# Kernel tuning notes

Measured on AMD Instinct MI355X. Metric: run time of the kernel, lower is better.

## Reference

```python
import jax, jax.numpy as jnp
import numpy as np

DIM = 2048
INNER = 8192
EPS_RMS = 1e-6
EPS_Q = 1e-5


def simple_rms_norm(x, dim):
    # x / sqrt(mean(x^2) + eps) * dim**-0.5
    rms = jnp.sqrt(jnp.mean(x * x, axis=-1, keepdims=True) + EPS_RMS)
    return x / rms * (dim ** -0.5)


def activation_quant(x):
    # per-token 8-bit quant over the last dim
    scale = 127.0 / jnp.clip(jnp.max(jnp.abs(x), axis=-1, keepdims=True), EPS_Q)
    return jnp.clip(jnp.round(x * scale), -128, 127) / scale


def weight_quant(w):
    # sign(w) * E[|w|]  (ternary since sign(0)=0)
    return jnp.sign(w) * jnp.mean(jnp.abs(w))


def bit_linear(x, w, b, dim_in):
    x_norm = simple_rms_norm(x, dim_in)
    x_q = activation_quant(x_norm)   # forward value (STE only matters for grads)
    w_q = weight_quant(w)
    return jnp.einsum('bsd,od->bso', x_q, w_q) + b


def setup_inputs() -> dict:
    key = jax.random.key(0)
    k1, k2, k3, k4, k5 = jax.random.split(key, 5)
    bound1 = 1.0 / np.sqrt(DIM)
    bound2 = 1.0 / np.sqrt(INNER)
    return {
        'x': jax.random.normal(k1, (4, 2048, DIM), dtype=jnp.float32),
        'w1': jax.random.uniform(k2, (INNER, DIM), jnp.float32, -bound1, bound1),
        'b1': jax.random.uniform(k3, (INNER,), jnp.float32, -bound1, bound1),
        'w2': jax.random.uniform(k4, (DIM, INNER), jnp.float32, -bound2, bound2),
        'b2': jax.random.uniform(k5, (DIM,), jnp.float32, -bound2, bound2),
    }


def reference(x, w1, b1, w2, b2):
    h = bit_linear(x, w1, b1, DIM)
    h = jax.nn.gelu(h, approximate=False)  # torch nn.GELU default = exact erf
    return bit_linear(h, w2, b2, INNER)
```

## Files before the change

### kernel.cpp

```cpp
#include <hip/hip_runtime.h>
#include <math.h>

#define TOK    8192
#define DIMK   2048
#define INNERK 8192

typedef __attribute__((ext_vector_type(4))) int i32x4;

__device__ __forceinline__ void gload_lds16(const void* g, void* l) {
  __builtin_amdgcn_global_load_lds(
      (const __attribute__((address_space(1))) unsigned int*)g,
      (__attribute__((address_space(3))) unsigned int*)l,
      16, 0, 0);
}

__global__ void wquant_kernel(const float* __restrict__ w, signed char* __restrict__ s,
                              double* __restrict__ sum_out) {
  const long n = (long)INNERK * DIMK;
  const long stride = (long)gridDim.x * blockDim.x * 4;
  double acc = 0.0;
  for (long i = ((long)blockIdx.x * blockDim.x + threadIdx.x) * 4; i < n; i += stride) {
    float4 v = *reinterpret_cast<const float4*>(w + i);
    char4 sc;
    sc.x = (signed char)((v.x > 0.f) - (v.x < 0.f));
    sc.y = (signed char)((v.y > 0.f) - (v.y < 0.f));
    sc.z = (signed char)((v.z > 0.f) - (v.z < 0.f));
    sc.w = (signed char)((v.w > 0.f) - (v.w < 0.f));
    *reinterpret_cast<char4*>(s + i) = sc;
    acc += (double)(fabsf(v.x) + fabsf(v.y) + fabsf(v.z) + fabsf(v.w));
  }
  for (int off = 32; off > 0; off >>= 1) acc += __shfl_down(acc, off, 64);
  __shared__ double red[4];
  const int lane = threadIdx.x & 63, wid = threadIdx.x >> 6;
  if (lane == 0) red[wid] = acc;
  __syncthreads();
  if (threadIdx.x == 0) atomicAdd(sum_out, red[0] + red[1] + red[2] + red[3]);
}

__device__ __forceinline__ signed char quant1(float x, float k, float scale) {
  float xn = x * k;
  int qi = (int)rintf(xn * scale);
  qi = qi < -128 ? -128 : (qi > 127 ? 127 : qi);
  return (signed char)qi;
}

template<int D, int VPT>
__global__ void actquant_kernel(const float* __restrict__ in, signed char* __restrict__ q,
                                float* __restrict__ invs, float cdim) {
  const int t = blockIdx.x;
  const float* row = in + (long)t * D;
  float4 v[VPT];
  float ss = 0.f, mx = 0.f;
#pragma unroll
  for (int j = 0; j < VPT; ++j) {
    v[j] = *reinterpret_cast<const float4*>(row + (j * 256 + threadIdx.x) * 4);
    ss += v[j].x * v[j].x + v[j].y * v[j].y + v[j].z * v[j].z + v[j].w * v[j].w;
    mx = fmaxf(mx, fmaxf(fmaxf(fabsf(v[j].x), fabsf(v[j].y)),
                         fmaxf(fabsf(v[j].z), fabsf(v[j].w))));
  }
  for (int off = 32; off > 0; off >>= 1) {
    ss += __shfl_down(ss, off, 64);
    mx = fmaxf(mx, __shfl_down(mx, off, 64));
  }
  __shared__ float rss[4], rmx[4];
  __shared__ float sh_k, sh_scale;
  const int lane = threadIdx.x & 63, wid = threadIdx.x >> 6;
  if (lane == 0) { rss[wid] = ss; rmx[wid] = mx; }
  __syncthreads();
  if (threadIdx.x == 0) {
    float s2 = rss[0] + rss[1] + rss[2] + rss[3];
    float m2 = fmaxf(fmaxf(rmx[0], rmx[1]), fmaxf(rmx[2], rmx[3]));
    float rms = sqrtf(s2 * (1.0f / D) + 1e-6f);
    float k = cdim / rms;
    float maxc = fmaxf(m2 * k, 1e-5f);
    float scale = 127.0f / maxc;
    sh_k = k; sh_scale = scale;
    invs[t] = 1.0f / scale;
  }
  __syncthreads();
  const float k = sh_k, scale = sh_scale;
#pragma unroll
  for (int j = 0; j < VPT; ++j) {
    char4 c;
    c.x = quant1(v[j].x, k, scale);
    c.y = quant1(v[j].y, k, scale);
    c.z = quant1(v[j].z, k, scale);
    c.w = quant1(v[j].w, k, scale);
    *reinterpret_cast<char4*>(q + (long)t * D + (j * 256 + threadIdx.x) * 4) = c;
  }
}

template<bool GELU>
__global__ __launch_bounds__(256) void gemm_i8_kernel(
    const signed char* __restrict__ A, const signed char* __restrict__ B,
    const float* __restrict__ bias, const float* __restrict__ invs,
    const double* __restrict__ wsum, float* __restrict__ C,
    int M, int N, int K)
{
  __shared__ alignas(16) signed char lA[128 * 128];
  __shared__ alignas(16) signed char lB[128 * 128];
  const int tid = threadIdx.x;
  const int lane = tid & 63, wid = tid >> 6;
  const long row0 = (long)blockIdx.x * 128;
  const long col0 = (long)blockIdx.y * 128;
  const int wr = (wid >> 1) * 64, wc = (wid & 1) * 64;

  const int srow  = lane >> 3;
  const int sslot = (lane & 7) ^ srow;
  const signed char* Ag = A + (row0 + wid * 32 + srow) * (long)K + (sslot << 4);
  const signed char* Bg = B + (col0 + wid * 32 + srow) * (long)K + (sslot << 4);
  signed char* lAw = lA + wid * 4096;
  signed char* lBw = lB + wid * 4096;

  i32x4 acc[4][4];
#pragma unroll
  for (int i = 0; i < 4; ++i)
#pragma unroll
    for (int j = 0; j < 4; ++j) acc[i][j] = (i32x4){0, 0, 0, 0};

  const int r15 = lane & 15, kg = lane >> 4;

  for (int k0 = 0; k0 < K; k0 += 128) {
#pragma unroll
    for (int i = 0; i < 4; ++i) {
      gload_lds16(Ag + (long)i * 8 * K + k0, lAw + i * 1024);
      gload_lds16(Bg + (long)i * 8 * K + k0, lBw + i * 1024);
    }
    __syncthreads();
#pragma unroll
    for (int s = 0; s < 2; ++s) {
      i32x4 af[4], bf[4];
#pragma unroll
      for (int m = 0; m < 4; ++m) {
        int row = wr + m * 16 + r15;
        int slot = (s * 4 + kg) ^ (row & 7);
        af[m] = *reinterpret_cast<const i32x4*>(lA + row * 128 + (slot << 4));
      }
#pragma unroll
      for (int n = 0; n < 4; ++n) {
        int row = wc + n * 16 + r15;
        int slot = (s * 4 + kg) ^ (row & 7);
        bf[n] = *reinterpret_cast<const i32x4*>(lB + row * 128 + (slot << 4));
      }
#pragma unroll
      for (int m = 0; m < 4; ++m)
#pragma unroll
        for (int n = 0; n < 4; ++n)
          acc[m][n] = __builtin_amdgcn_mfma_i32_16x16x64_i8(af[m], bf[n], acc[m][n], 0, 0, 0);
    }
    __syncthreads();
  }

  const float mval = (float)(wsum[0] * (1.0 / 16777216.0));
#pragma unroll
  for (int m = 0; m < 4; ++m) {
    const int rb = wr + m * 16 + kg * 4;
#pragma unroll
    for (int r = 0; r < 4; ++r) {
      const long grow = row0 + rb + r;
      const float as = mval * invs[grow];
#pragma unroll
      for (int n = 0; n < 4; ++n) {
        const long gcol = col0 + wc + n * 16 + r15;
        float v = (float)acc[m][n][r] * as + bias[gcol];
        if (GELU) v = 0.5f * v * (1.0f + erff(v * 0.70710678118654752f));
        C[grow * N + gcol] = v;
      }
    }
  }
}

extern "C" void kernel_launch(void* const* d_in, const int* in_sizes, int n_in,
                              void* d_out, int out_size, void* d_ws, size_t ws_size,
                              hipStream_t stream) {
  const float* x  = (const float*)d_in[0];
  const float* w1 = (const float*)d_in[1];
  const float* b1 = (const float*)d_in[2];
  const float* w2 = (const float*)d_in[3];
  const float* b2 = (const float*)d_in[4];
  float* out = (float*)d_out;

  char* ws = (char*)d_ws;
  double* wsum      = (double*)ws;
  float*  inv1      = (float*)(ws + 1024);
  float*  inv2      = (float*)(ws + 1024 + 32768);
  signed char* s1   = (signed char*)(ws + 66560);
  signed char* s2   = s1 + (long)INNERK * DIMK;
  signed char* qx   = s2 + (long)INNERK * DIMK;
  signed char* qh   = qx + (long)TOK * DIMK;
  float* hg         = (float*)(qh + (long)TOK * INNERK);

  const long fixed = 66560 + 3L * 16777216L + 67108864L;
  long avail = (long)ws_size - fixed;
  long chunk = avail / ((long)INNERK * 4);
  if (chunk > TOK) chunk = TOK;
  chunk &= ~127L;
  if (chunk < 128) chunk = 128;

  hipMemsetAsync(d_ws, 0, 1024, stream);
  hipLaunchKernelGGL(wquant_kernel, dim3(2048), dim3(256), 0, stream, w1, s1, wsum);
  hipLaunchKernelGGL(wquant_kernel, dim3(2048), dim3(256), 0, stream, w2, s2, wsum + 1);
  hipLaunchKernelGGL((actquant_kernel<DIMK, 2>), dim3(TOK), dim3(256), 0, stream,
                     x, qx, inv1, 0.022097086912079608f);
  for (long t0 = 0; t0 < TOK; t0 += chunk) {
    long mt = TOK - t0 < chunk ? TOK - t0 : chunk;
    hipLaunchKernelGGL((gemm_i8_kernel<true>), dim3(mt / 128, INNERK / 128), dim3(256), 0, stream,
                       qx + t0 * DIMK, s1, b1, inv1 + t0, wsum, hg,
                       (int)mt, INNERK, DIMK);
    hipLaunchKernelGGL((actquant_kernel<INNERK, 8>), dim3(mt), dim3(256), 0, stream,
                       hg, qh + t0 * INNERK, inv2 + t0, 0.011048543456039804f);
  }
  hipLaunchKernelGGL((gemm_i8_kernel<false>), dim3(TOK / 128, DIMK / 128), dim3(256), 0, stream,
                     qh, s2, b2, inv2, wsum + 1, out, TOK, DIMK, INNERK);
}
```

Baseline: 710.3 us.

## Rewrite int8 GEMM as 256x256 double-buffered 8-wave pipelined kernel with XCD swizzle

```diff
diff --git a/kernel.cpp b/kernel.cpp
--- a/kernel.cpp
+++ b/kernel.cpp
@@ -14,8 +14,11 @@
       16, 0, 0);
 }
 
-__global__ void wquant_kernel(const float* __restrict__ w, signed char* __restrict__ s,
-                              double* __restrict__ sum_out) {
+__global__ void wquant_kernel(const float* __restrict__ w1, const float* __restrict__ w2,
+                              signed char* __restrict__ s1, signed char* __restrict__ s2,
+                              double* __restrict__ sums) {
+  const float* w = blockIdx.y ? w2 : w1;
+  signed char* s = blockIdx.y ? s2 : s1;
   const long n = (long)INNERK * DIMK;
   const long stride = (long)gridDim.x * blockDim.x * 4;
   double acc = 0.0;
@@ -34,7 +37,7 @@
   const int lane = threadIdx.x & 63, wid = threadIdx.x >> 6;
   if (lane == 0) red[wid] = acc;
   __syncthreads();
-  if (threadIdx.x == 0) atomicAdd(sum_out, red[0] + red[1] + red[2] + red[3]);
+  if (threadIdx.x == 0) atomicAdd(&sums[blockIdx.y], red[0] + red[1] + red[2] + red[3]);
 }
 
 __device__ __forceinline__ signed char quant1(float x, float k, float scale) {
@@ -91,83 +94,135 @@
 }
 
 template<bool GELU>
-__global__ __launch_bounds__(256) void gemm_i8_kernel(
+__global__ __launch_bounds__(512, 2) void gemm_i8_8p(
     const signed char* __restrict__ A, const signed char* __restrict__ B,
     const float* __restrict__ bias, const float* __restrict__ invs,
     const double* __restrict__ wsum, float* __restrict__ C,
-    int M, int N, int K)
+    int M, int N, int K, int MB)
 {
-  __shared__ alignas(16) signed char lA[128 * 128];
-  __shared__ alignas(16) signed char lB[128 * 128];
-  const int tid = threadIdx.x;
+  __shared__ alignas(16) signed char lA[2][256][128];
+  __shared__ alignas(16) signed char lB[2][256][128];
+
+  const int tid  = threadIdx.x;
   const int lane = tid & 63, wid = tid >> 6;
-  const long row0 = (long)blockIdx.x * 128;
-  const long col0 = (long)blockIdx.y * 128;
-  const int wr = (wid >> 1) * 64, wc = (wid & 1) * 64;
-
-  const int srow  = lane >> 3;
-  const int sslot = (lane & 7) ^ srow;
-  const signed char* Ag = A + (row0 + wid * 32 + srow) * (long)K + (sslot << 4);
-  const signed char* Bg = B + (col0 + wid * 32 + srow) * (long)K + (sslot << 4);
-  signed char* lAw = lA + wid * 4096;
-  signed char* lBw = lB + wid * 4096;
-
-  i32x4 acc[4][4];
-#pragma unroll
-  for (int i = 0; i < 4; ++i)
-#pragma unroll
-    for (int j = 0; j < 4; ++j) acc[i][j] = (i32x4){0, 0, 0, 0};
-
+  const int wr = wid >> 2, wc = wid & 3;
   const int r15 = lane & 15, kg = lane >> 4;
 
-  for (int k0 = 0; k0 < K; k0 += 128) {
-#pragma unroll
-    for (int i = 0; i < 4; ++i) {
-      gload_lds16(Ag + (long)i * 8 * K + k0, lAw + i * 1024);
-      gload_lds16(Bg + (long)i * 8 * K + k0, lBw + i * 1024);
-    }
-    __syncthreads();
-#pragma unroll
-    for (int s = 0; s < 2; ++s) {
-      i32x4 af[4], bf[4];
-#pragma unroll
-      for (int m = 0; m < 4; ++m) {
-        int row = wr + m * 16 + r15;
-        int slot = (s * 4 + kg) ^ (row & 7);
-        af[m] = *reinterpret_cast<const i32x4*>(lA + row * 128 + (slot << 4));
-      }
+  const int nwg = gridDim.x, cpx = nwg >> 3;
+  const int sid = ((int)blockIdx.x & 7) * cpx + ((int)blockIdx.x >> 3);
+  const int bm = sid % MB, bn = sid / MB;
+  const long row0 = (long)bm * 256, col0 = (long)bn * 256;
+
+  const int srow = tid >> 3;
+  const int scol = ((tid & 7) ^ (srow & 7)) << 4;
+  const signed char* Abase = A + (row0 + srow) * (long)K + scol;
+  const signed char* Bbase = B + (col0 + srow) * (long)K + scol;
+  char* lAw = (char*)&lA[0][0][0] + wid * 1024;
+  char* lBw = (char*)&lB[0][0][0] + wid * 1024;
+
+#define STAGE_A(bb, hh, tt) do {                                               \
+    const signed char* _g = Abase + (long)(hh) * 128 * K + (long)(tt) * 128;   \
+    gload_lds16(_g,                lAw + (bb) * 32768 + (hh) * 16384);         \
+    gload_lds16(_g + 64 * (long)K, lAw + (bb) * 32768 + (hh) * 16384 + 8192);  \
+  } while (0)
+#define STAGE_B(bb, hh, tt) do {                                               \
+    const signed char* _g = Bbase + (long)(hh) * 128 * K + (long)(tt) * 128;   \
+    gload_lds16(_g,                lBw + (bb) * 32768 + (hh) * 16384);         \
+    gload_lds16(_g + 64 * (long)K, lBw + (bb) * 32768 + (hh) * 16384 + 8192);  \
+  } while (0)
+
+  i32x4 acc[8][4];
+#pragma unroll
+  for (int m = 0; m < 8; ++m)
+#pragma unroll
+    for (int n = 0; n < 4; ++n) acc[m][n] = (i32x4){0, 0, 0, 0};
+
+  i32x4 af[4][2], bf[2][2];
+  const int rdk = r15 & 7;
+  const int sl0 = (kg ^ rdk) << 4;
+  const int sl1 = ((4 + kg) ^ rdk) << 4;
+  const int arow0 = wr * 16 + r15;
+  const int brow0 = wc * 16 + r15;
+
+#define LD_A(bb, Ah) do {                                                      \
+    _Pragma("unroll") for (int i = 0; i < 4; ++i) {                            \
+      const char* _p = (const char*)&lA[bb][(Ah) * 128 + i * 32 + arow0][0];   \
+      af[i][0] = *(const i32x4*)(_p + sl0);                                    \
+      af[i][1] = *(const i32x4*)(_p + sl1);                                    \
+    } } while (0)
+#define LD_B(bb, Bh) do {                                                      \
+    _Pragma("unroll") for (int j = 0; j < 2; ++j) {                            \
+      const char* _p = (const char*)&lB[bb][(Bh) * 128 + j * 64 + brow0][0];   \
+      bf[j][0] = *(const i32x4*)(_p + sl0);                                    \
+      bf[j][1] = *(const i32x4*)(_p + sl1);                                    \
+    } } while (0)
+
+#define MFMA16(Ah, Bh) do {                                                    \
+    __builtin_amdgcn_s_setprio(1);                                             \
+    _Pragma("unroll") for (int ks = 0; ks < 2; ++ks)                           \
+    _Pragma("unroll") for (int i = 0; i < 4; ++i)                              \
+    _Pragma("unroll") for (int j = 0; j < 2; ++j)                              \
+      acc[(Ah) * 4 + i][(Bh) * 2 + j] = __builtin_amdgcn_mfma_i32_16x16x64_i8( \
+          af[i][ks], bf[j][ks], acc[(Ah) * 4 + i][(Bh) * 2 + j], 0, 0, 0);     \
+    __builtin_amdgcn_s_setprio(0);                                             \
+  } while (0)
+
+#define BAR() do { asm volatile("" ::: "memory");                              \
+    __builtin_amdgcn_s_barrier(); asm volatile("" ::: "memory"); } while (0)
+
+  STAGE_A(0, 0, 0); STAGE_B(0, 0, 0); STAGE_A(0, 1, 0); STAGE_B(0, 1, 0);
+
+  const int T = K >> 7;
+  for (int t = 0; t < T; ++t) {
+    const int b = t & 1, nb = b ^ 1;
+    const bool nlast = (t != T - 1);
+    asm volatile("s_waitcnt vmcnt(4)" ::: "memory");
+    BAR();
+    LD_A(b, 0); LD_B(b, 0);
+    if (nlast) STAGE_A(nb, 0, t + 1);
+    MFMA16(0, 0);
+    if (nlast) asm volatile("s_waitcnt vmcnt(4)" ::: "memory");
+    else       asm volatile("s_waitcnt vmcnt(2)" ::: "memory");
+    BAR();
+    LD_A(b, 1);
+    if (nlast) STAGE_B(nb, 0, t + 1);
+    MFMA16(1, 0);
+    if (nlast) asm volatile("s_waitcnt vmcnt(4)" ::: "memory");
+    else       asm volatile("s_waitcnt vmcnt(0)" ::: "memory");
+    BAR();
+    LD_B(b, 1);
+    if (nlast) STAGE_A(nb, 1, t + 1);
+    MFMA16(1, 1);
+    LD_A(b, 0);
+    if (nlast) STAGE_B(nb, 1, t + 1);
+    MFMA16(0, 1);
+  }
+
+  const float mval = (float)(wsum[0] * (1.0 / 16777216.0));
+#pragma unroll
+  for (int m = 0; m < 8; ++m) {
+    const int Ah = m >> 2, im = m & 3;
+    const long rowb = row0 + Ah * 128 + im * 32 + wr * 16 + kg * 4;
+#pragma unroll
+    for (int r = 0; r < 4; ++r) {
+      const long grow = rowb + r;
+      const float as = mval * invs[grow];
+      float* crow = C + grow * N + col0;
 #pragma unroll
       for (int n = 0; n < 4; ++n) {
-        int row = wc + n * 16 + r15;
-        int slot = (s * 4 + kg) ^ (row & 7);
-        bf[n] = *reinterpret_cast<const i32x4*>(lB + row * 128 + (slot << 4));
-      }
-#pragma unroll
-      for (int m = 0; m < 4; ++m)
-#pragma unroll
-        for (int n = 0; n < 4; ++n)
-          acc[m][n] = __builtin_amdgcn_mfma_i32_16x16x64_i8(af[m], bf[n], acc[m][n], 0, 0, 0);
-    }
-    __syncthreads();
-  }
-
-  const float mval = (float)(wsum[0] * (1.0 / 16777216.0));
-#pragma unroll
-  for (int m = 0; m < 4; ++m) {
-    const int rb = wr + m * 16 + kg * 4;
-#pragma unroll
-    for (int r = 0; r < 4; ++r) {
-      const long grow = row0 + rb + r;
-      const float as = mval * invs[grow];
-#pragma unroll
-      for (int n = 0; n < 4; ++n) {
-        const long gcol = col0 + wc + n * 16 + r15;
-        float v = (float)acc[m][n][r] * as + bias[gcol];
+        const int gcol = (n >> 1) * 128 + (n & 1) * 64 + wc * 16 + r15;
+        float v = (float)acc[m][n][r] * as + bias[col0 + gcol];
         if (GELU) v = 0.5f * v * (1.0f + erff(v * 0.70710678118654752f));
-        C[grow * N + gcol] = v;
+        crow[gcol] = v;
       }
     }
   }
+#undef STAGE_A
+#undef STAGE_B
+#undef LD_A
+#undef LD_B
+#undef MFMA16
+#undef BAR
 }
 
 extern "C" void kernel_launch(void* const* d_in, const int* in_sizes, int n_in,
@@ -194,22 +249,22 @@
   long avail = (long)ws_size - fixed;
   long chunk = avail / ((long)INNERK * 4);
   if (chunk > TOK) chunk = TOK;
-  chunk &= ~127L;
-  if (chunk < 128) chunk = 128;
+  chunk &= ~255L;
+  if (chunk < 256) chunk = 256;
 
   hipMemsetAsync(d_ws, 0, 1024, stream);
-  hipLaunchKernelGGL(wquant_kernel, dim3(2048), dim3(256), 0, stream, w1, s1, wsum);
-  hipLaunchKernelGGL(wquant_kernel, dim3(2048), dim3(256), 0, stream, w2, s2, wsum + 1);
+  hipLaunchKernelGGL(wquant_kernel, dim3(2048, 2), dim3(256), 0, stream,
+                     w1, w2, s1, s2, wsum);
   hipLaunchKernelGGL((actquant_kernel<DIMK, 2>), dim3(TOK), dim3(256), 0, stream,
                      x, qx, inv1, 0.022097086912079608f);
   for (long t0 = 0; t0 < TOK; t0 += chunk) {
     long mt = TOK - t0 < chunk ? TOK - t0 : chunk;
-    hipLaunchKernelGGL((gemm_i8_kernel<true>), dim3(mt / 128, INNERK / 128), dim3(256), 0, stream,
+    hipLaunchKernelGGL((gemm_i8_8p<true>), dim3((mt / 256) * (INNERK / 256)), dim3(512), 0, stream,
                        qx + t0 * DIMK, s1, b1, inv1 + t0, wsum, hg,
-                       (int)mt, INNERK, DIMK);
+                       (int)mt, INNERK, DIMK, (int)(mt / 256));
     hipLaunchKernelGGL((actquant_kernel<INNERK, 8>), dim3(mt), dim3(256), 0, stream,
                        hg, qh + t0 * INNERK, inv2 + t0, 0.011048543456039804f);
   }
-  hipLaunchKernelGGL((gemm_i8_kernel<false>), dim3(TOK / 128, DIMK / 128), dim3(256), 0, stream,
-                     qh, s2, b2, inv2, wsum + 1, out, TOK, DIMK, INNERK);
-}
+  hipLaunchKernelGGL((gemm_i8_8p<false>), dim3((TOK / 256) * (DIMK / 256)), dim3(512), 0, stream,
+                     qh, s2, b2, inv2, wsum + 1, out, TOK, DIMK, INNERK, TOK / 256);
+}
```

After: 672.5 us. -5.3%, faster.
